# Performance work log

Hardware: AMD Instinct MI355X
Metric: run time of the kernel (lower is better)

Reference implementation:

```python
import jax, jax.numpy as jnp
import numpy as np

EPS = 1e-3  # Keras LayerNormalization default epsilon


def layernorm(x, g, b):
    mu = jnp.mean(x, axis=-1, keepdims=True)
    var = jnp.var(x, axis=-1, keepdims=True)
    return (x - mu) * jax.lax.rsqrt(var + EPS) * g + b


def setup_inputs() -> dict:
    key = jax.random.key(0)
    ks = jax.random.split(key, 16)
    B, T, C = 2, 2048, 1024
    F = 4 * C
    std = 0.02
    inp = {
        "x": jax.random.normal(ks[0], (B, T, C), jnp.float32),
        "ln1_g": jnp.ones((C,), jnp.float32),
        "ln1_b": jnp.zeros((C,), jnp.float32),
        "Wq": std * jax.random.normal(ks[1], (C, C), jnp.float32),
        "bq": jnp.zeros((C,), jnp.float32),
        "Wk": std * jax.random.normal(ks[2], (C, C), jnp.float32),
        "bk": jnp.zeros((C,), jnp.float32),
        "Wv": std * jax.random.normal(ks[3], (C, C), jnp.float32),
        "bv": jnp.zeros((C,), jnp.float32),
        "ln2_g": jnp.ones((C,), jnp.float32),
        "ln2_b": jnp.zeros((C,), jnp.float32),
        "W1": std * jax.random.normal(ks[4], (C, F), jnp.float32),
        "b1": jnp.zeros((F,), jnp.float32),
        "W2": std * jax.random.normal(ks[5], (F, C), jnp.float32),
        "b2": jnp.zeros((C,), jnp.float32),
    }
    return inp


N_HEADS = 16


def reference(x, ln1_g, ln1_b, Wq, bq, Wk, bk, Wv, bv, ln2_g, ln2_b, W1, b1, W2, b2):
    B, T, C = x.shape
    H = N_HEADS
    D = C // H

    h = layernorm(x, ln1_g, ln1_b)
    # [B,T,C] -> [B,H,T,D]
    def split_heads(y):
        return y.reshape(B, T, H, D).transpose(0, 2, 1, 3)

    q = split_heads(h @ Wq + bq)
    k = split_heads(h @ Wk + bk)
    v = split_heads(h @ Wv + bv)

    # Faithful to original: scores = K @ Q^T, i.e. scores[i,j] = k_i . q_j
    scores = jnp.einsum("bhid,bhjd->bhij", k, q) / jnp.sqrt(jnp.float32(D))
    causal = jnp.tril(jnp.ones((T, T), bool))  # [T,T]
    scores = jnp.where(causal[None, None], scores, -jnp.inf)
    w = jax.nn.softmax(scores, axis=-1)
    attn = jnp.einsum("bhij,bhjd->bhid", w, v)  # [B,H,T,D]
    attn = attn.transpose(0, 2, 1, 3).reshape(B, T, C)
    x = x + attn

    h2 = layernorm(x, ln2_g, ln2_b)
    ffn = jax.nn.gelu(h2 @ W1 + b1, approximate=False) @ W2 + b2
    x = x + ffn
    return x
```

## Files before the change

### kernel.cpp

```cpp
#include <hip/hip_runtime.h>
#include <hip/hip_bf16.h>
#include <math.h>

typedef __hip_bfloat16 bf16;
typedef __attribute__((ext_vector_type(8))) short bf16x8;
typedef __attribute__((ext_vector_type(4))) float f32x4;

__device__ __forceinline__ unsigned short f2bf_rne(float f) {
  unsigned u = __float_as_uint(f);
  u += 0x7fffu + ((u >> 16) & 1u);
  return (unsigned short)(u >> 16);
}
__device__ __forceinline__ float bf2f(unsigned short s) {
  return __uint_as_float(((unsigned)s) << 16);
}

__device__ __forceinline__ float gelu_fast(float v) {
  float u = v * (0.7978845608f + 0.0356774081f * v * v);
  float t = __builtin_amdgcn_exp2f(u * 2.8853900818f);
  float r = __builtin_amdgcn_rcpf(t + 1.0f);
  return v - v * r;
}

#define GLOBAL_AS __attribute__((address_space(1)))
#define LDS_AS __attribute__((address_space(3)))
__device__ __forceinline__ void gl2lds16(const void* g, void* l) {
  __builtin_amdgcn_global_load_lds((const GLOBAL_AS void*)g, (LDS_AS void*)l, 16, 0, 0);
}

__global__ __launch_bounds__(256) void ln_kernel(const float* __restrict__ x,
                                                 const float* __restrict__ g,
                                                 const float* __restrict__ b,
                                                 bf16* __restrict__ h) {
  int row = blockIdx.x, t = threadIdx.x;
  const float4 xv = ((const float4*)(x + (size_t)row * 1024))[t];
  float s = xv.x + xv.y + xv.z + xv.w;
  float sq = xv.x * xv.x + xv.y * xv.y + xv.z * xv.z + xv.w * xv.w;
  #pragma unroll
  for (int m = 1; m < 64; m <<= 1) { s += __shfl_xor(s, m); sq += __shfl_xor(sq, m); }
  __shared__ float ps[4], pq[4];
  if ((t & 63) == 0) { ps[t >> 6] = s; pq[t >> 6] = sq; }
  __syncthreads();
  s = ps[0] + ps[1] + ps[2] + ps[3];
  sq = pq[0] + pq[1] + pq[2] + pq[3];
  float mean = s * (1.0f / 1024.0f);
  float var = sq * (1.0f / 1024.0f) - mean * mean;
  float rs = rsqrtf(var + 1e-3f);
  float4 gv = ((const float4*)g)[t];
  float4 bv = ((const float4*)b)[t];
  ushort4 o;
  o.x = f2bf_rne((xv.x - mean) * rs * gv.x + bv.x);
  o.y = f2bf_rne((xv.y - mean) * rs * gv.y + bv.y);
  o.z = f2bf_rne((xv.z - mean) * rs * gv.z + bv.z);
  o.w = f2bf_rne((xv.w - mean) * rs * gv.w + bv.w);
  ((ushort4*)(h + (size_t)row * 1024))[t] = o;
}

__device__ __forceinline__ void tr_tile(const float* __restrict__ W, bf16* __restrict__ WT,
                                        int R, int Cc, int bx, int by, int t) {
  __shared__ float tile[32][33];
  int tx = t & 31, ty = t >> 5;
  #pragma unroll
  for (int k = 0; k < 4; k++) {
    int rr = ty + k * 8;
    tile[rr][tx] = W[(size_t)(by + rr) * Cc + bx + tx];
  }
  __syncthreads();
  unsigned short* out = reinterpret_cast<unsigned short*>(WT);
  #pragma unroll
  for (int k = 0; k < 4; k++) {
    int rr = ty + k * 8;
    out[(size_t)(bx + rr) * R + by + tx] = f2bf_rne(tile[tx][rr]);
  }
}

__global__ __launch_bounds__(256) void transpose_all(const float* __restrict__ Wq,
                                                     const float* __restrict__ Wk,
                                                     const float* __restrict__ Wv,
                                                     const float* __restrict__ W1,
                                                     const float* __restrict__ W2,
                                                     bf16* __restrict__ WqkT,
                                                     bf16* __restrict__ W1T,
                                                     bf16* __restrict__ W2T) {
  int id = blockIdx.x, t = threadIdx.x;
  if (id < 3072) {
    int sect = id >> 10, r = id & 1023;
    const float* W = sect == 0 ? Wq : (sect == 1 ? Wk : Wv);
    bf16* WT = WqkT + (size_t)sect * 1048576;
    tr_tile(W, WT, 1024, 1024, (r & 31) * 32, (r >> 5) * 32, t);
  } else if (id < 7168) {
    int r = id - 3072;
    tr_tile(W1, W1T, 1024, 4096, (r & 127) * 32, (r >> 7) * 32, t);
  } else {
    int r = id - 7168;
    tr_tile(W2, W2T, 4096, 1024, (r & 31) * 32, (r >> 5) * 32, t);
  }
}

__device__ __forceinline__ void mainloop_256(const bf16* __restrict__ A,
                                             const bf16* __restrict__ BT,
                                             int lda, int nk, int m0, int n0,
                                             char* ldsb, int t,
                                             f32x4 (&acc)[8][4]) {
  const int lane = t & 63, wave = t >> 6;
  const int l = lane & 15, quad = lane >> 4;
  const int wm = (wave >> 2) * 128, wn = (wave & 3) * 64;
  const int srow = wave * 8 + (lane >> 3);
  const int scol = ((lane & 7) ^ (lane >> 3)) * 8;
  const int grp0 = (quad ^ (l & 7)) * 16;
  const int grp1 = ((4 + quad) ^ (l & 7)) * 16;

  bf16x8 a[4][2], b01[2][2], b23[2][2];

  auto stA = [&](int buf, int half, int kt) {
    const bf16* s = A + (size_t)(m0 + half * 128 + srow) * lda + kt * 64 + scol;
    char* d = ldsb + buf * 65536 + half * 16384 + wave * 1024;
    gl2lds16(s, d);
    gl2lds16(s + (size_t)64 * lda, d + 8192);
  };
  auto stB = [&](int buf, int half, int kt) {
    const bf16* s = BT + (size_t)(n0 + half * 128 + srow) * lda + kt * 64 + scol;
    char* d = ldsb + buf * 65536 + 32768 + half * 16384 + wave * 1024;
    gl2lds16(s, d);
    gl2lds16(s + (size_t)64 * lda, d + 8192);
  };
  auto rdA = [&](int buf, int mh) {
    const char* base = ldsb + buf * 65536 + (wm + mh * 64 + l) * 128;
    #pragma unroll
    for (int ii = 0; ii < 4; ii++) {
      a[ii][0] = *(const bf16x8*)(base + ii * 2048 + grp0);
      a[ii][1] = *(const bf16x8*)(base + ii * 2048 + grp1);
    }
  };
  auto rdB = [&](int buf, int nh, bf16x8 (&bb)[2][2]) {
    const char* base = ldsb + buf * 65536 + 32768 + (wn + nh * 32 + l) * 128;
    #pragma unroll
    for (int jj = 0; jj < 2; jj++) {
      bb[jj][0] = *(const bf16x8*)(base + jj * 2048 + grp0);
      bb[jj][1] = *(const bf16x8*)(base + jj * 2048 + grp1);
    }
  };
  auto mm4 = [&](int mi, bf16x8 (&bb)[2][2], int nj) {
    #pragma unroll
    for (int ii = 0; ii < 4; ii++)
      #pragma unroll
      for (int jj = 0; jj < 2; jj++) {
        acc[mi + ii][nj + jj] = __builtin_amdgcn_mfma_f32_16x16x32_bf16(
            a[ii][0], bb[jj][0], acc[mi + ii][nj + jj], 0, 0, 0);
        acc[mi + ii][nj + jj] = __builtin_amdgcn_mfma_f32_16x16x32_bf16(
            a[ii][1], bb[jj][1], acc[mi + ii][nj + jj], 0, 0, 0);
      }
  };

#define BARX() __builtin_amdgcn_s_barrier()
#define LGKM0() do { asm volatile("s_waitcnt lgkmcnt(0)" ::: "memory"); \
                     __builtin_amdgcn_sched_barrier(0); } while (0)
#define HALF4(BC, DOA, SAB, SAK, DOB, SBB, SBK, VMN)                      \
  do {                                                                    \
    rdA(BC, 0); rdB(BC, 0, b01);                                          \
    if (DOA) stA(SAB, 0, SAK);                                            \
    BARX(); LGKM0();                                                      \
    __builtin_amdgcn_s_setprio(1); mm4(0, b01, 0);                        \
    __builtin_amdgcn_s_setprio(0); BARX();                                \
    rdB(BC, 1, b23);                                                      \
    if (DOA) stA(SAB, 1, SAK);                                            \
    BARX(); LGKM0();                                                      \
    __builtin_amdgcn_s_setprio(1); mm4(0, b23, 2);                        \
    __builtin_amdgcn_s_setprio(0); BARX();                                \
    rdA(BC, 1);                                                           \
    if (DOB) stB(SBB, 0, SBK);                                            \
    BARX(); LGKM0();                                                      \
    __builtin_amdgcn_s_setprio(1); mm4(4, b01, 0);                        \
    __builtin_amdgcn_s_setprio(0); BARX();                                \
    if (DOB) stB(SBB, 1, SBK);                                            \
    BARX();                                                               \
    __builtin_amdgcn_s_setprio(1); mm4(4, b23, 2);                        \
    __builtin_amdgcn_s_setprio(0);                                        \
    asm volatile("s_waitcnt vmcnt(" VMN ")" ::: "memory");                \
    BARX();                                                               \
  } while (0)

  const int nt = nk >> 6;
  stA(0, 0, 0); stA(0, 1, 0);
  stB(0, 0, 0); stB(0, 1, 0);
  stB(1, 0, 1); stB(1, 1, 1);
  asm volatile("s_waitcnt vmcnt(4)" ::: "memory");
  BARX();
  int tt = 0;
  for (; tt + 2 < nt; tt += 2) {
    HALF4(0, 1, 1, tt + 1, 1, 0, tt + 2, "4");
    HALF4(1, 1, 0, tt + 2, 1, 1, tt + 3, "4");
  }
  HALF4(0, 1, 1, tt + 1, 0, 0, 0, "0");
  HALF4(1, 0, 0, 0, 0, 0, 0, "0");
#undef HALF4
#undef LGKM0
#undef BARX
}

__global__ __launch_bounds__(512, 2) void gemm_ffn1(const bf16* __restrict__ A,
                                                    const bf16* __restrict__ BT,
                                                    const float* __restrict__ bias,
                                                    bf16* __restrict__ out,
                                                    int N, int K) {
  extern __shared__ char lds[];
  int t = threadIdx.x;
  int n0 = blockIdx.x * 256, m0 = blockIdx.y * 256;
  f32x4 acc[8][4];
  #pragma unroll
  for (int i = 0; i < 8; i++)
    #pragma unroll
    for (int j = 0; j < 4; j++) acc[i][j] = (f32x4){0.f, 0.f, 0.f, 0.f};
  mainloop_256(A, BT, K, K, m0, n0, lds, t, acc);

  int lane = t & 63, wave = t >> 6;
  int l = lane & 15, quad = lane >> 4;
  int wm = (wave >> 2) * 128, wn = (wave & 3) * 64;
  int r4 = quad * 4;
  unsigned short* os = reinterpret_cast<unsigned short*>(out);
  #pragma unroll
  for (int i = 0; i < 8; i++)
    #pragma unroll
    for (int j = 0; j < 4; j++) {
      int col = n0 + wn + j * 16 + l;
      float bval = bias[col];
      #pragma unroll
      for (int r = 0; r < 4; r++) {
        int row = m0 + wm + i * 16 + r4 + r;
        os[(size_t)row * N + col] = f2bf_rne(gelu_fast(acc[i][j][r] + bval));
      }
    }
}

__global__ __launch_bounds__(512, 2) void gemm_ffn2(const bf16* __restrict__ A,
                                                    const bf16* __restrict__ BT,
                                                    unsigned short* __restrict__ p0,
                                                    unsigned short* __restrict__ p1,
                                                    unsigned short* __restrict__ p2,
                                                    unsigned short* __restrict__ p3) {
  extern __shared__ char lds[];
  int t = threadIdx.x;
  int n0 = blockIdx.x * 256, m0 = blockIdx.y * 256;
  int z = blockIdx.z;
  f32x4 acc[8][4];
  #pragma unroll
  for (int i = 0; i < 8; i++)
    #pragma unroll
    for (int j = 0; j < 4; j++) acc[i][j] = (f32x4){0.f, 0.f, 0.f, 0.f};
  mainloop_256(A + z * 1024, BT + z * 1024, 4096, 1024, m0, n0, lds, t, acc);

  unsigned short* p = z == 0 ? p0 : (z == 1 ? p1 : (z == 2 ? p2 : p3));
  int lane = t & 63, wave = t >> 6;
  int l = lane & 15, quad = lane >> 4;
  int wm = (wave >> 2) * 128, wn = (wave & 3) * 64;
  int r4 = quad * 4;
  #pragma unroll
  for (int i = 0; i < 8; i++)
    #pragma unroll
    for (int j = 0; j < 4; j++) {
      int col = n0 + wn + j * 16 + l;
      #pragma unroll
      for (int r = 0; r < 4; r++) {
        int row = m0 + wm + i * 16 + r4 + r;
        p[(size_t)row * 1024 + col] = f2bf_rne(acc[i][j][r]);
      }
    }
}

__global__ __launch_bounds__(256) void reduce_ffn2(const unsigned short* __restrict__ p0,
                                                   const unsigned short* __restrict__ p1,
                                                   const unsigned short* __restrict__ p2,
                                                   const unsigned short* __restrict__ p3,
                                                   const float* __restrict__ x1,
                                                   const float* __restrict__ bias,
                                                   float* __restrict__ out) {
  int row = blockIdx.x, t = threadIdx.x;
  size_t base = (size_t)row * 1024;
  ushort4 a = ((const ushort4*)(p0 + base))[t];
  ushort4 b = ((const ushort4*)(p1 + base))[t];
  ushort4 c = ((const ushort4*)(p2 + base))[t];
  ushort4 d = ((const ushort4*)(p3 + base))[t];
  float4 xv = ((const float4*)(x1 + base))[t];
  float4 bv = ((const float4*)bias)[t];
  float4 o;
  o.x = (bf2f(a.x) + bf2f(b.x)) + (bf2f(c.x) + bf2f(d.x)) + xv.x + bv.x;
  o.y = (bf2f(a.y) + bf2f(b.y)) + (bf2f(c.y) + bf2f(d.y)) + xv.y + bv.y;
  o.z = (bf2f(a.z) + bf2f(b.z)) + (bf2f(c.z) + bf2f(d.z)) + xv.z + bv.z;
  o.w = (bf2f(a.w) + bf2f(b.w)) + (bf2f(c.w) + bf2f(d.w)) + xv.w + bv.w;
  ((float4*)(out + base))[t] = o;
}

__global__ __launch_bounds__(512, 2) void gemm_qkv(const bf16* __restrict__ A,
                                                   const bf16* __restrict__ BT,
                                                   const float* __restrict__ bq,
                                                   const float* __restrict__ bk,
                                                   const float* __restrict__ bv,
                                                   bf16* __restrict__ qb,
                                                   bf16* __restrict__ kb,
                                                   bf16* __restrict__ vt,
                                                   int K) {
  extern __shared__ char lds[];
  int t = threadIdx.x;
  int n0 = blockIdx.x * 256, m0 = blockIdx.y * 256;
  f32x4 acc[8][4];
  #pragma unroll
  for (int i = 0; i < 8; i++)
    #pragma unroll
    for (int j = 0; j < 4; j++) acc[i][j] = (f32x4){0.f, 0.f, 0.f, 0.f};
  mainloop_256(A, BT, K, K, m0, n0, lds, t, acc);

  int lane = t & 63, wave = t >> 6;
  int l = lane & 15, quad = lane >> 4;
  int wm = (wave >> 2) * 128, wn = (wave & 3) * 64;
  int sect = n0 >> 10;
  const float* bias = sect == 0 ? bq : (sect == 1 ? bk : bv);
  int r4 = quad * 4;
  #pragma unroll
  for (int i = 0; i < 8; i++)
    #pragma unroll
    for (int j = 0; j < 4; j++) {
      int col = n0 + wn + j * 16 + l;
      int c1 = col & 1023;
      float bval = bias[c1];
      int row0 = m0 + wm + i * 16 + r4;
      if (sect < 2) {
        bf16* o = sect == 0 ? qb : kb;
        unsigned short* os = reinterpret_cast<unsigned short*>(o);
        #pragma unroll
        for (int r = 0; r < 4; r++)
          os[(size_t)(row0 + r) * 1024 + c1] = f2bf_rne(acc[i][j][r] + bval);
      } else {
        int hh = c1 >> 6, d = c1 & 63;
        int b = row0 >> 11, t0 = row0 & 2047;
        ushort4 pk;
        pk.x = f2bf_rne(acc[i][j][0] + bval);
        pk.y = f2bf_rne(acc[i][j][1] + bval);
        pk.z = f2bf_rne(acc[i][j][2] + bval);
        pk.w = f2bf_rne(acc[i][j][3] + bval);
        *(ushort4*)((unsigned short*)vt + (size_t)((b * 16 + hh) * 64 + d) * 2048 + t0) = pk;
      }
    }
}

__global__ __launch_bounds__(256) void attn_mfma(const bf16* __restrict__ qb,
                                                 const bf16* __restrict__ kb,
                                                 const bf16* __restrict__ vt,
                                                 const float* __restrict__ x,
                                                 float* __restrict__ x1) {
  __shared__ bf16 QP[64][72];
  __shared__ bf16 KV[2][2][64][64];
  int t = threadIdx.x;
  int bh = blockIdx.x;
  int b = bh >> 4, h = bh & 15;
  size_t qk_base = (size_t)b * 2048 * 1024 + (size_t)h * 64;
  size_t vt_base = (size_t)bh * 64 * 2048;
  int lane = t & 63, wave = t >> 6;
  int l = lane & 15, quad = lane >> 4;
  int sw = l & 7;
  int srow8 = lane >> 3;
  int scol = ((lane & 7) ^ srow8) * 8;
  const float cs = 0.125f * 1.44269504088896f;
  int y = blockIdx.y;

  for (int pass = 0; pass < 2; pass++) {
    int it = pass ? 31 - y : y;
    int i0 = it * 64;
    int njt = it + 1;
    __syncthreads();
    #pragma unroll
    for (int c0 = 0; c0 < 512; c0 += 256) {
      int c = c0 + t;
      int row = c >> 3, col8 = (c & 7) * 8;
      *(uint4*)&QP[row][col8] = *(const uint4*)(kb + qk_base + (size_t)(i0 + row) * 1024 + col8);
    }
    #pragma unroll
    for (int c = 0; c < 2; c++) {
      int rr = wave * 16 + c * 8 + srow8;
      gl2lds16(qb + qk_base + (size_t)rr * 1024 + scol,
               (char*)KV + wave * 2048 + c * 1024);
      gl2lds16(vt + vt_base + (size_t)rr * 2048 + scol,
               (char*)KV + 8192 + wave * 2048 + c * 1024);
    }
    __syncthreads();

    bf16x8 qf0 = *(const bf16x8*)&QP[wave * 16 + l][quad * 8];
    bf16x8 qf1 = *(const bf16x8*)&QP[wave * 16 + l][32 + quad * 8];
    float lsum = 0.f;
    f32x4 Oacc[4];
    #pragma unroll
    for (int dt = 0; dt < 4; dt++) Oacc[dt] = (f32x4){0.f, 0.f, 0.f, 0.f};
    int iblk = i0 + wave * 16;

    int buf = 0;
    for (int jt = 0; jt < njt; jt++) {
      int j0v = jt * 64;
      if (jt + 1 < njt) {
        int j1 = j0v + 64;
        #pragma unroll
        for (int c = 0; c < 2; c++) {
          int rr = wave * 16 + c * 8 + srow8;
          gl2lds16(qb + qk_base + (size_t)(j1 + rr) * 1024 + scol,
                   (char*)KV + (buf ^ 1) * 16384 + wave * 2048 + c * 1024);
          gl2lds16(vt + vt_base + (size_t)rr * 2048 + j1 + scol,
                   (char*)KV + (buf ^ 1) * 16384 + 8192 + wave * 2048 + c * 1024);
        }
      }

      const bf16* Kb = &KV[buf][0][0][0];
      #pragma unroll
      for (int nt = 0; nt < 4; nt++) {
        int jb = j0v + nt * 16;
        uint2 pk;
        if (jb > iblk + 15) {
          pk.x = 0u; pk.y = 0u;
        } else {
          const bf16* kr = Kb + (nt * 16 + l) * 64;
          bf16x8 kf0 = *(const bf16x8*)(kr + ((quad ^ sw) * 8));
          bf16x8 kf1 = *(const bf16x8*)(kr + (((4 + quad) ^ sw) * 8));
          f32x4 sv = (f32x4){0.f, 0.f, 0.f, 0.f};
          sv = __builtin_amdgcn_mfma_f32_16x16x32_bf16(kf0, qf0, sv, 0, 0, 0);
          sv = __builtin_amdgcn_mfma_f32_16x16x32_bf16(kf1, qf1, sv, 0, 0, 0);
          float p0, p1, p2, p3;
          if (jb + 15 <= iblk) {
            p0 = __builtin_amdgcn_exp2f(sv[0] * cs);
            p1 = __builtin_amdgcn_exp2f(sv[1] * cs);
            p2 = __builtin_amdgcn_exp2f(sv[2] * cs);
            p3 = __builtin_amdgcn_exp2f(sv[3] * cs);
          } else {
            int i_ = iblk + l, jbase = jb + quad * 4;
            p0 = (jbase + 0 > i_) ? 0.f : __builtin_amdgcn_exp2f(sv[0] * cs);
            p1 = (jbase + 1 > i_) ? 0.f : __builtin_amdgcn_exp2f(sv[1] * cs);
            p2 = (jbase + 2 > i_) ? 0.f : __builtin_amdgcn_exp2f(sv[2] * cs);
            p3 = (jbase + 3 > i_) ? 0.f : __builtin_amdgcn_exp2f(sv[3] * cs);
          }
          lsum += (p0 + p1) + (p2 + p3);
          union { __hip_bfloat162 h2; unsigned u; } c0u, c1u;
          c0u.h2 = __float22bfloat162_rn(make_float2(p0, p1));
          c1u.h2 = __float22bfloat162_rn(make_float2(p2, p3));
          pk.x = c0u.u; pk.y = c1u.u;
        }
        *(uint2*)&QP[wave * 16 + l][nt * 16 + quad * 4] = pk;
      }
      asm volatile("s_waitcnt lgkmcnt(0)" ::: "memory");

      bf16x8 ap0 = *(const bf16x8*)&QP[wave * 16 + l][quad * 8];
      bf16x8 ap1 = *(const bf16x8*)&QP[wave * 16 + l][32 + quad * 8];
      const bf16* Vb = &KV[buf][1][0][0];
      #pragma unroll
      for (int dt = 0; dt < 4; dt++) {
        const bf16* vr = Vb + (dt * 16 + l) * 64;
        bf16x8 bv0 = *(const bf16x8*)(vr + ((quad ^ sw) * 8));
        bf16x8 bv1 = *(const bf16x8*)(vr + (((4 + quad) ^ sw) * 8));
        Oacc[dt] = __builtin_amdgcn_mfma_f32_16x16x32_bf16(ap0, bv0, Oacc[dt], 0, 0, 0);
        Oacc[dt] = __builtin_amdgcn_mfma_f32_16x16x32_bf16(ap1, bv1, Oacc[dt], 0, 0, 0);
      }
      __syncthreads();
      buf ^= 1;
    }

    lsum += __shfl_xor(lsum, 16);
    lsum += __shfl_xor(lsum, 32);
    #pragma unroll
    for (int r = 0; r < 4; r++) {
      float lv = __shfl(lsum, quad * 4 + r);
      float inv = 1.0f / lv;
      int row = i0 + wave * 16 + quad * 4 + r;
      size_t gi = qk_base + (size_t)row * 1024;
      #pragma unroll
      for (int dt = 0; dt < 4; dt++) {
        int d = dt * 16 + l;
        x1[gi + d] = x[gi + d] + Oacc[dt][r] * inv;
      }
    }
  }
}

extern "C" void kernel_launch(void* const* d_in, const int* in_sizes, int n_in,
                              void* d_out, int out_size, void* d_ws, size_t ws_size,
                              hipStream_t stream) {
  const float* x    = (const float*)d_in[0];
  const float* ln1g = (const float*)d_in[1];
  const float* ln1b = (const float*)d_in[2];
  const float* Wq   = (const float*)d_in[3];
  const float* bq   = (const float*)d_in[4];
  const float* Wk   = (const float*)d_in[5];
  const float* bk   = (const float*)d_in[6];
  const float* Wv   = (const float*)d_in[7];
  const float* bv   = (const float*)d_in[8];
  const float* ln2g = (const float*)d_in[9];
  const float* ln2b = (const float*)d_in[10];
  const float* W1   = (const float*)d_in[11];
  const float* b1   = (const float*)d_in[12];
  const float* W2   = (const float*)d_in[13];
  const float* b2   = (const float*)d_in[14];

  char* ws = (char*)d_ws;
  float* x1  = (float*)(ws + 0);
  bf16* h    = (bf16*)(ws + 16777216);
  bf16* WqkT = (bf16*)(ws + 25165824);
  bf16* W1T  = (bf16*)(ws + 31457280);
  bf16* W2T  = (bf16*)(ws + 39845888);
  bf16* qb   = (bf16*)(ws + 48234496);
  bf16* kb   = (bf16*)(ws + 56623104);
  bf16* vt   = (bf16*)(ws + 65011712);
  bf16* act  = (bf16*)(ws + 73400320);

  static bool s_attr_done = false;
  if (!s_attr_done) {
    hipFuncSetAttribute(reinterpret_cast<const void*>(gemm_qkv),
                        hipFuncAttributeMaxDynamicSharedMemorySize, 131072);
    hipFuncSetAttribute(reinterpret_cast<const void*>(gemm_ffn1),
                        hipFuncAttributeMaxDynamicSharedMemorySize, 131072);
    hipFuncSetAttribute(reinterpret_cast<const void*>(gemm_ffn2),
                        hipFuncAttributeMaxDynamicSharedMemorySize, 131072);
    s_attr_done = true;
  }

  transpose_all<<<11264, 256, 0, stream>>>(Wq, Wk, Wv, W1, W2, WqkT, W1T, W2T);
  ln_kernel<<<4096, 256, 0, stream>>>(x, ln1g, ln1b, h);
  gemm_qkv<<<dim3(12, 16), 512, 131072, stream>>>(h, WqkT, bq, bk, bv, qb, kb, vt, 1024);
  attn_mfma<<<dim3(32, 16), 256, 0, stream>>>(qb, kb, vt, x, x1);
  ln_kernel<<<4096, 256, 0, stream>>>(x1, ln2g, ln2b, h);
  gemm_ffn1<<<dim3(16, 16), 512, 131072, stream>>>(h, W1T, b1, act, 4096, 1024);
  gemm_ffn2<<<dim3(4, 16, 4), 512, 131072, stream>>>(act, W2T,
      (unsigned short*)qb, (unsigned short*)kb, (unsigned short*)vt, (unsigned short*)h);
  reduce_ffn2<<<4096, 256, 0, stream>>>((const unsigned short*)qb, (const unsigned short*)kb,
                                        (const unsigned short*)vt, (const unsigned short*)h,
                                        x1, b2, (float*)d_out);
}
```

Before: 291.4 us.

## Run both attention passes concurrently in 512-thread blocks, reading K/V from global

The attention kernel now uses 512 threads, so its two query-tile passes (y and 31-y) run concurrently in separate wave groups instead of one after another. The shared K/V double buffer and every block-wide barrier are gone. Each wave loads K and V fragments straight from global memory (relying on L1/L2) and keeps only a private P tile in LDS. On the diagonal tile, waves skip the upper-half V MFMA that is fully masked. The trade is more global-load traffic and cache pressure in exchange for no synchronisation, and the loads are no longer staged with a swizzle.

```diff
diff --git a/kernel.cpp b/kernel.cpp
--- a/kernel.cpp
+++ b/kernel.cpp
@@ -342,13 +342,12 @@
     }
 }
 
-__global__ __launch_bounds__(256) void attn_mfma(const bf16* __restrict__ qb,
-                                                 const bf16* __restrict__ kb,
-                                                 const bf16* __restrict__ vt,
-                                                 const float* __restrict__ x,
-                                                 float* __restrict__ x1) {
-  __shared__ bf16 QP[64][72];
-  __shared__ bf16 KV[2][2][64][64];
+__global__ __launch_bounds__(512, 4) void attn_mfma(const bf16* __restrict__ qb,
+                                                    const bf16* __restrict__ kb,
+                                                    const bf16* __restrict__ vt,
+                                                    const float* __restrict__ x,
+                                                    float* __restrict__ x1) {
+  __shared__ bf16 P[8][16][68];
   int t = threadIdx.x;
   int bh = blockIdx.x;
   int b = bh >> 4, h = bh & 15;
@@ -356,121 +355,98 @@
   size_t vt_base = (size_t)bh * 64 * 2048;
   int lane = t & 63, wave = t >> 6;
   int l = lane & 15, quad = lane >> 4;
-  int sw = l & 7;
-  int srow8 = lane >> 3;
-  int scol = ((lane & 7) ^ srow8) * 8;
   const float cs = 0.125f * 1.44269504088896f;
   int y = blockIdx.y;
-
-  for (int pass = 0; pass < 2; pass++) {
-    int it = pass ? 31 - y : y;
-    int i0 = it * 64;
-    int njt = it + 1;
-    __syncthreads();
-    #pragma unroll
-    for (int c0 = 0; c0 < 512; c0 += 256) {
-      int c = c0 + t;
-      int row = c >> 3, col8 = (c & 7) * 8;
-      *(uint4*)&QP[row][col8] = *(const uint4*)(kb + qk_base + (size_t)(i0 + row) * 1024 + col8);
-    }
-    #pragma unroll
-    for (int c = 0; c < 2; c++) {
-      int rr = wave * 16 + c * 8 + srow8;
-      gl2lds16(qb + qk_base + (size_t)rr * 1024 + scol,
-               (char*)KV + wave * 2048 + c * 1024);
-      gl2lds16(vt + vt_base + (size_t)rr * 2048 + scol,
-               (char*)KV + 8192 + wave * 2048 + c * 1024);
-    }
-    __syncthreads();
-
-    bf16x8 qf0 = *(const bf16x8*)&QP[wave * 16 + l][quad * 8];
-    bf16x8 qf1 = *(const bf16x8*)&QP[wave * 16 + l][32 + quad * 8];
-    float lsum = 0.f;
-    f32x4 Oacc[4];
-    #pragma unroll
-    for (int dt = 0; dt < 4; dt++) Oacc[dt] = (f32x4){0.f, 0.f, 0.f, 0.f};
-    int iblk = i0 + wave * 16;
-
-    int buf = 0;
-    for (int jt = 0; jt < njt; jt++) {
-      int j0v = jt * 64;
-      if (jt + 1 < njt) {
-        int j1 = j0v + 64;
-        #pragma unroll
-        for (int c = 0; c < 2; c++) {
-          int rr = wave * 16 + c * 8 + srow8;
-          gl2lds16(qb + qk_base + (size_t)(j1 + rr) * 1024 + scol,
-                   (char*)KV + (buf ^ 1) * 16384 + wave * 2048 + c * 1024);
-          gl2lds16(vt + vt_base + (size_t)rr * 2048 + j1 + scol,
-                   (char*)KV + (buf ^ 1) * 16384 + 8192 + wave * 2048 + c * 1024);
+  int half = wave >> 2, w4 = wave & 3;
+  int it = half ? 31 - y : y;
+  int i0 = it * 64;
+  int iblk = i0 + w4 * 16;
+  int njt = it + 1;
+
+  const bf16* qrow = kb + qk_base + (size_t)(iblk + l) * 1024;
+  bf16x8 qf0 = *(const bf16x8*)(qrow + quad * 8);
+  bf16x8 qf1 = *(const bf16x8*)(qrow + 32 + quad * 8);
+
+  float lsum = 0.f;
+  f32x4 Oacc[4];
+  #pragma unroll
+  for (int dt = 0; dt < 4; dt++) Oacc[dt] = (f32x4){0.f, 0.f, 0.f, 0.f};
+
+  bf16 (*Pw)[68] = P[wave];
+
+  for (int jt = 0; jt < njt; jt++) {
+    int j0v = jt * 64;
+    const bf16* Kb = qb + qk_base + (size_t)j0v * 1024;
+    #pragma unroll
+    for (int nt = 0; nt < 4; nt++) {
+      int jb = j0v + nt * 16;
+      uint2 pk;
+      if (jb > iblk + 15) {
+        pk.x = 0u; pk.y = 0u;
+      } else {
+        const bf16* kr = Kb + (size_t)(nt * 16 + l) * 1024;
+        bf16x8 kf0 = *(const bf16x8*)(kr + quad * 8);
+        bf16x8 kf1 = *(const bf16x8*)(kr + 32 + quad * 8);
+        f32x4 sv = (f32x4){0.f, 0.f, 0.f, 0.f};
+        sv = __builtin_amdgcn_mfma_f32_16x16x32_bf16(kf0, qf0, sv, 0, 0, 0);
+        sv = __builtin_amdgcn_mfma_f32_16x16x32_bf16(kf1, qf1, sv, 0, 0, 0);
+        float p0, p1, p2, p3;
+        if (jb + 15 <= iblk) {
+          p0 = __builtin_amdgcn_exp2f(sv[0] * cs);
+          p1 = __builtin_amdgcn_exp2f(sv[1] * cs);
+          p2 = __builtin_amdgcn_exp2f(sv[2] * cs);
+          p3 = __builtin_amdgcn_exp2f(sv[3] * cs);
+        } else {
+          int i_ = iblk + l, jbase = jb + quad * 4;
+          p0 = (jbase + 0 > i_) ? 0.f : __builtin_amdgcn_exp2f(sv[0] * cs);
+          p1 = (jbase + 1 > i_) ? 0.f : __builtin_amdgcn_exp2f(sv[1] * cs);
+          p2 = (jbase + 2 > i_) ? 0.f : __builtin_amdgcn_exp2f(sv[2] * cs);
+          p3 = (jbase + 3 > i_) ? 0.f : __builtin_amdgcn_exp2f(sv[3] * cs);
         }
-      }
-
-      const bf16* Kb = &KV[buf][0][0][0];
-      #pragma unroll
-      for (int nt = 0; nt < 4; nt++) {
-        int jb = j0v + nt * 16;
-        uint2 pk;
-        if (jb > iblk + 15) {
-          pk.x = 0u; pk.y = 0u;
-        } else {
-          const bf16* kr = Kb + (nt * 16 + l) * 64;
-          bf16x8 kf0 = *(const bf16x8*)(kr + ((quad ^ sw) * 8));
-          bf16x8 kf1 = *(const bf16x8*)(kr + (((4 + quad) ^ sw) * 8));
-          f32x4 sv = (f32x4){0.f, 0.f, 0.f, 0.f};
-          sv = __builtin_amdgcn_mfma_f32_16x16x32_bf16(kf0, qf0, sv, 0, 0, 0);
-          sv = __builtin_amdgcn_mfma_f32_16x16x32_bf16(kf1, qf1, sv, 0, 0, 0);
-          float p0, p1, p2, p3;
-          if (jb + 15 <= iblk) {
-            p0 = __builtin_amdgcn_exp2f(sv[0] * cs);
-            p1 = __builtin_amdgcn_exp2f(sv[1] * cs);
-            p2 = __builtin_amdgcn_exp2f(sv[2] * cs);
-            p3 = __builtin_amdgcn_exp2f(sv[3] * cs);
-          } else {
-            int i_ = iblk + l, jbase = jb + quad * 4;
-            p0 = (jbase + 0 > i_) ? 0.f : __builtin_amdgcn_exp2f(sv[0] * cs);
-            p1 = (jbase + 1 > i_) ? 0.f : __builtin_amdgcn_exp2f(sv[1] * cs);
-            p2 = (jbase + 2 > i_) ? 0.f : __builtin_amdgcn_exp2f(sv[2] * cs);
-            p3 = (jbase + 3 > i_) ? 0.f : __builtin_amdgcn_exp2f(sv[3] * cs);
-          }
-          lsum += (p0 + p1) + (p2 + p3);
-          union { __hip_bfloat162 h2; unsigned u; } c0u, c1u;
-          c0u.h2 = __float22bfloat162_rn(make_float2(p0, p1));
-          c1u.h2 = __float22bfloat162_rn(make_float2(p2, p3));
-          pk.x = c0u.u; pk.y = c1u.u;
-        }
-        *(uint2*)&QP[wave * 16 + l][nt * 16 + quad * 4] = pk;
-      }
-      asm volatile("s_waitcnt lgkmcnt(0)" ::: "memory");
-
-      bf16x8 ap0 = *(const bf16x8*)&QP[wave * 16 + l][quad * 8];
-      bf16x8 ap1 = *(const bf16x8*)&QP[wave * 16 + l][32 + quad * 8];
-      const bf16* Vb = &KV[buf][1][0][0];
+        lsum += (p0 + p1) + (p2 + p3);
+        union { __hip_bfloat162 h2; unsigned u; } c0u, c1u;
+        c0u.h2 = __float22bfloat162_rn(make_float2(p0, p1));
+        c1u.h2 = __float22bfloat162_rn(make_float2(p2, p3));
+        pk.x = c0u.u; pk.y = c1u.u;
+      }
+      *(uint2*)&Pw[l][nt * 16 + quad * 4] = pk;
+    }
+    asm volatile("s_waitcnt lgkmcnt(0)" ::: "memory");
+
+    bf16x8 ap0 = *(const bf16x8*)&Pw[l][quad * 8];
+    const bf16* Vb = vt + vt_base + j0v;
+    if ((jt < it) || (w4 >= 2)) {
+      bf16x8 ap1 = *(const bf16x8*)&Pw[l][32 + quad * 8];
       #pragma unroll
       for (int dt = 0; dt < 4; dt++) {
-        const bf16* vr = Vb + (dt * 16 + l) * 64;
-        bf16x8 bv0 = *(const bf16x8*)(vr + ((quad ^ sw) * 8));
-        bf16x8 bv1 = *(const bf16x8*)(vr + (((4 + quad) ^ sw) * 8));
+        const bf16* vr = Vb + (size_t)(dt * 16 + l) * 2048;
+        bf16x8 bv0 = *(const bf16x8*)(vr + quad * 8);
+        bf16x8 bv1 = *(const bf16x8*)(vr + 32 + quad * 8);
         Oacc[dt] = __builtin_amdgcn_mfma_f32_16x16x32_bf16(ap0, bv0, Oacc[dt], 0, 0, 0);
         Oacc[dt] = __builtin_amdgcn_mfma_f32_16x16x32_bf16(ap1, bv1, Oacc[dt], 0, 0, 0);
       }
-      __syncthreads();
-      buf ^= 1;
-    }
-
-    lsum += __shfl_xor(lsum, 16);
-    lsum += __shfl_xor(lsum, 32);
-    #pragma unroll
-    for (int r = 0; r < 4; r++) {
-      float lv = __shfl(lsum, quad * 4 + r);
-      float inv = 1.0f / lv;
-      int row = i0 + wave * 16 + quad * 4 + r;
-      size_t gi = qk_base + (size_t)row * 1024;
+    } else {
       #pragma unroll
       for (int dt = 0; dt < 4; dt++) {
-        int d = dt * 16 + l;
-        x1[gi + d] = x[gi + d] + Oacc[dt][r] * inv;
-      }
+        const bf16* vr = Vb + (size_t)(dt * 16 + l) * 2048;
+        bf16x8 bv0 = *(const bf16x8*)(vr + quad * 8);
+        Oacc[dt] = __builtin_amdgcn_mfma_f32_16x16x32_bf16(ap0, bv0, Oacc[dt], 0, 0, 0);
+      }
+    }
+  }
+
+  lsum += __shfl_xor(lsum, 16);
+  lsum += __shfl_xor(lsum, 32);
+  #pragma unroll
+  for (int r = 0; r < 4; r++) {
+    float lv = __shfl(lsum, quad * 4 + r);
+    float inv = 1.0f / lv;
+    int row = iblk + quad * 4 + r;
+    size_t gi = qk_base + (size_t)row * 1024;
+    #pragma unroll
+    for (int dt = 0; dt < 4; dt++) {
+      int d = dt * 16 + l;
+      x1[gi + d] = x[gi + d] + Oacc[dt][r] * inv;
     }
   }
 }
@@ -519,7 +495,7 @@
   transpose_all<<<11264, 256, 0, stream>>>(Wq, Wk, Wv, W1, W2, WqkT, W1T, W2T);
   ln_kernel<<<4096, 256, 0, stream>>>(x, ln1g, ln1b, h);
   gemm_qkv<<<dim3(12, 16), 512, 131072, stream>>>(h, WqkT, bq, bk, bv, qb, kb, vt, 1024);
-  attn_mfma<<<dim3(32, 16), 256, 0, stream>>>(qb, kb, vt, x, x1);
+  attn_mfma<<<dim3(32, 16), 512, 0, stream>>>(qb, kb, vt, x, x1);
   ln_kernel<<<4096, 256, 0, stream>>>(x1, ln2g, ln2b, h);
   gemm_ffn1<<<dim3(16, 16), 512, 131072, stream>>>(h, W1T, b1, act, 4096, 1024);
   gemm_ffn2<<<dim3(4, 16, 4), 512, 131072, stream>>>(act, W2T,
```

Measured after the change: 374.7 us. +28.6%, slower.

## Split attention row-tile pairs into separate blocks with heavy-first ordering and swizzled LDS

Applied to the files above, without the earlier changes.

Previously each attention block processed two query tiles (it and 31-it) in sequence for load balance. Now each block handles one tile, launched on a 32x32 grid, with the mapping ordering long causal tiles first so heavy blocks start early. The Q/P shared buffer drops its padding and uses an XOR swizzle, Q is loaded with async global-to-LDS copies, and launch bounds request 4 blocks per CU for higher occupancy. The cost is more blocks with uneven work, relying on the scheduler to balance them.

```diff
diff --git a/kernel.cpp b/kernel.cpp
--- a/kernel.cpp
+++ b/kernel.cpp
@@ -342,12 +342,12 @@
     }
 }
 
-__global__ __launch_bounds__(256) void attn_mfma(const bf16* __restrict__ qb,
-                                                 const bf16* __restrict__ kb,
-                                                 const bf16* __restrict__ vt,
-                                                 const float* __restrict__ x,
-                                                 float* __restrict__ x1) {
-  __shared__ bf16 QP[64][72];
+__global__ __launch_bounds__(256, 4) void attn_mfma(const bf16* __restrict__ qb,
+                                                    const bf16* __restrict__ kb,
+                                                    const bf16* __restrict__ vt,
+                                                    const float* __restrict__ x,
+                                                    float* __restrict__ x1) {
+  __shared__ bf16 QP[64][64];
   __shared__ bf16 KV[2][2][64][64];
   int t = threadIdx.x;
   int bh = blockIdx.x;
@@ -361,116 +361,113 @@
   int scol = ((lane & 7) ^ srow8) * 8;
   const float cs = 0.125f * 1.44269504088896f;
   int y = blockIdx.y;
-
-  for (int pass = 0; pass < 2; pass++) {
-    int it = pass ? 31 - y : y;
-    int i0 = it * 64;
-    int njt = it + 1;
+  int yr = y & 7, yk = y >> 3;
+  int it = yk == 0 ? 31 - yr : (yk == 1 ? 16 + yr : (yk == 2 ? 15 - yr : yr));
+  int i0 = it * 64;
+  int njt = it + 1;
+  int iblk = i0 + wave * 16;
+
+  #pragma unroll
+  for (int c = 0; c < 2; c++) {
+    int rr = wave * 16 + c * 8 + srow8;
+    gl2lds16(kb + qk_base + (size_t)(i0 + rr) * 1024 + scol,
+             (char*)QP + wave * 2048 + c * 1024);
+    gl2lds16(qb + qk_base + (size_t)rr * 1024 + scol,
+             (char*)KV + wave * 2048 + c * 1024);
+    gl2lds16(vt + vt_base + (size_t)rr * 2048 + scol,
+             (char*)KV + 8192 + wave * 2048 + c * 1024);
+  }
+  __syncthreads();
+
+  const char* qr = (const char*)&QP[wave * 16 + l][0];
+  bf16x8 qf0 = *(const bf16x8*)(qr + ((quad ^ sw) * 16));
+  bf16x8 qf1 = *(const bf16x8*)(qr + (((4 + quad) ^ sw) * 16));
+  float lsum = 0.f;
+  f32x4 Oacc[4];
+  #pragma unroll
+  for (int dt = 0; dt < 4; dt++) Oacc[dt] = (f32x4){0.f, 0.f, 0.f, 0.f};
+
+  char* Pw = (char*)&QP[wave * 16 + l][0];
+
+  int buf = 0;
+  for (int jt = 0; jt < njt; jt++) {
+    int j0v = jt * 64;
+    if (jt + 1 < njt) {
+      int j1 = j0v + 64;
+      #pragma unroll
+      for (int c = 0; c < 2; c++) {
+        int rr = wave * 16 + c * 8 + srow8;
+        gl2lds16(qb + qk_base + (size_t)(j1 + rr) * 1024 + scol,
+                 (char*)KV + (buf ^ 1) * 16384 + wave * 2048 + c * 1024);
+        gl2lds16(vt + vt_base + (size_t)rr * 2048 + j1 + scol,
+                 (char*)KV + (buf ^ 1) * 16384 + 8192 + wave * 2048 + c * 1024);
+      }
+    }
+
+    const bf16* Kb = &KV[buf][0][0][0];
+    #pragma unroll
+    for (int nt = 0; nt < 4; nt++) {
+      int jb = j0v + nt * 16;
+      uint2 pk;
+      if (jb > iblk + 15) {
+        pk.x = 0u; pk.y = 0u;
+      } else {
+        const bf16* kr = Kb + (nt * 16 + l) * 64;
+        bf16x8 kf0 = *(const bf16x8*)(kr + ((quad ^ sw) * 8));
+        bf16x8 kf1 = *(const bf16x8*)(kr + (((4 + quad) ^ sw) * 8));
+        f32x4 sv = (f32x4){0.f, 0.f, 0.f, 0.f};
+        sv = __builtin_amdgcn_mfma_f32_16x16x32_bf16(kf0, qf0, sv, 0, 0, 0);
+        sv = __builtin_amdgcn_mfma_f32_16x16x32_bf16(kf1, qf1, sv, 0, 0, 0);
+        float p0, p1, p2, p3;
+        if (jb + 15 <= iblk) {
+          p0 = __builtin_amdgcn_exp2f(sv[0] * cs);
+          p1 = __builtin_amdgcn_exp2f(sv[1] * cs);
+          p2 = __builtin_amdgcn_exp2f(sv[2] * cs);
+          p3 = __builtin_amdgcn_exp2f(sv[3] * cs);
+        } else {
+          int i_ = iblk + l, jbase = jb + quad * 4;
+          p0 = (jbase + 0 > i_) ? 0.f : __builtin_amdgcn_exp2f(sv[0] * cs);
+          p1 = (jbase + 1 > i_) ? 0.f : __builtin_amdgcn_exp2f(sv[1] * cs);
+          p2 = (jbase + 2 > i_) ? 0.f : __builtin_amdgcn_exp2f(sv[2] * cs);
+          p3 = (jbase + 3 > i_) ? 0.f : __builtin_amdgcn_exp2f(sv[3] * cs);
+        }
+        lsum += (p0 + p1) + (p2 + p3);
+        union { __hip_bfloat162 h2; unsigned u; } c0u, c1u;
+        c0u.h2 = __float22bfloat162_rn(make_float2(p0, p1));
+        c1u.h2 = __float22bfloat162_rn(make_float2(p2, p3));
+        pk.x = c0u.u; pk.y = c1u.u;
+      }
+      *(uint2*)(Pw + (((nt * 2 + (quad >> 1)) ^ sw) << 4) + ((quad & 1) << 3)) = pk;
+    }
+    asm volatile("s_waitcnt lgkmcnt(0)" ::: "memory");
+
+    bf16x8 ap0 = *(const bf16x8*)(Pw + ((quad ^ sw) << 4));
+    bf16x8 ap1 = *(const bf16x8*)(Pw + (((4 + quad) ^ sw) << 4));
+    const bf16* Vb = &KV[buf][1][0][0];
+    #pragma unroll
+    for (int dt = 0; dt < 4; dt++) {
+      const bf16* vr = Vb + (dt * 16 + l) * 64;
+      bf16x8 bv0 = *(const bf16x8*)(vr + ((quad ^ sw) * 8));
+      bf16x8 bv1 = *(const bf16x8*)(vr + (((4 + quad) ^ sw) * 8));
+      Oacc[dt] = __builtin_amdgcn_mfma_f32_16x16x32_bf16(ap0, bv0, Oacc[dt], 0, 0, 0);
+      Oacc[dt] = __builtin_amdgcn_mfma_f32_16x16x32_bf16(ap1, bv1, Oacc[dt], 0, 0, 0);
+    }
     __syncthreads();
-    #pragma unroll
-    for (int c0 = 0; c0 < 512; c0 += 256) {
-      int c = c0 + t;
-      int row = c >> 3, col8 = (c & 7) * 8;
-      *(uint4*)&QP[row][col8] = *(const uint4*)(kb + qk_base + (size_t)(i0 + row) * 1024 + col8);
-    }
-    #pragma unroll
-    for (int c = 0; c < 2; c++) {
-      int rr = wave * 16 + c * 8 + srow8;
-      gl2lds16(qb + qk_base + (size_t)rr * 1024 + scol,
-               (char*)KV + wave * 2048 + c * 1024);
-      gl2lds16(vt + vt_base + (size_t)rr * 2048 + scol,
-               (char*)KV + 8192 + wave * 2048 + c * 1024);
-    }
-    __syncthreads();
-
-    bf16x8 qf0 = *(const bf16x8*)&QP[wave * 16 + l][quad * 8];
-    bf16x8 qf1 = *(const bf16x8*)&QP[wave * 16 + l][32 + quad * 8];
-    float lsum = 0.f;
-    f32x4 Oacc[4];
-    #pragma unroll
-    for (int dt = 0; dt < 4; dt++) Oacc[dt] = (f32x4){0.f, 0.f, 0.f, 0.f};
-    int iblk = i0 + wave * 16;
-
-    int buf = 0;
-    for (int jt = 0; jt < njt; jt++) {
-      int j0v = jt * 64;
-      if (jt + 1 < njt) {
-        int j1 = j0v + 64;
-        #pragma unroll
-        for (int c = 0; c < 2; c++) {
-          int rr = wave * 16 + c * 8 + srow8;
-          gl2lds16(qb + qk_base + (size_t)(j1 + rr) * 1024 + scol,
-                   (char*)KV + (buf ^ 1) * 16384 + wave * 2048 + c * 1024);
-          gl2lds16(vt + vt_base + (size_t)rr * 2048 + j1 + scol,
-                   (char*)KV + (buf ^ 1) * 16384 + 8192 + wave * 2048 + c * 1024);
-        }
-      }
-
-      const bf16* Kb = &KV[buf][0][0][0];
-      #pragma unroll
-      for (int nt = 0; nt < 4; nt++) {
-        int jb = j0v + nt * 16;
-        uint2 pk;
-        if (jb > iblk + 15) {
-          pk.x = 0u; pk.y = 0u;
-        } else {
-          const bf16* kr = Kb + (nt * 16 + l) * 64;
-          bf16x8 kf0 = *(const bf16x8*)(kr + ((quad ^ sw) * 8));
-          bf16x8 kf1 = *(const bf16x8*)(kr + (((4 + quad) ^ sw) * 8));
-          f32x4 sv = (f32x4){0.f, 0.f, 0.f, 0.f};
-          sv = __builtin_amdgcn_mfma_f32_16x16x32_bf16(kf0, qf0, sv, 0, 0, 0);
-          sv = __builtin_amdgcn_mfma_f32_16x16x32_bf16(kf1, qf1, sv, 0, 0, 0);
-          float p0, p1, p2, p3;
-          if (jb + 15 <= iblk) {
-            p0 = __builtin_amdgcn_exp2f(sv[0] * cs);
-            p1 = __builtin_amdgcn_exp2f(sv[1] * cs);
-            p2 = __builtin_amdgcn_exp2f(sv[2] * cs);
-            p3 = __builtin_amdgcn_exp2f(sv[3] * cs);
-          } else {
-            int i_ = iblk + l, jbase = jb + quad * 4;
-            p0 = (jbase + 0 > i_) ? 0.f : __builtin_amdgcn_exp2f(sv[0] * cs);
-            p1 = (jbase + 1 > i_) ? 0.f : __builtin_amdgcn_exp2f(sv[1] * cs);
-            p2 = (jbase + 2 > i_) ? 0.f : __builtin_amdgcn_exp2f(sv[2] * cs);
-            p3 = (jbase + 3 > i_) ? 0.f : __builtin_amdgcn_exp2f(sv[3] * cs);
-          }
-          lsum += (p0 + p1) + (p2 + p3);
-          union { __hip_bfloat162 h2; unsigned u; } c0u, c1u;
-          c0u.h2 = __float22bfloat162_rn(make_float2(p0, p1));
-          c1u.h2 = __float22bfloat162_rn(make_float2(p2, p3));
-          pk.x = c0u.u; pk.y = c1u.u;
-        }
-        *(uint2*)&QP[wave * 16 + l][nt * 16 + quad * 4] = pk;
-      }
-      asm volatile("s_waitcnt lgkmcnt(0)" ::: "memory");
-
-      bf16x8 ap0 = *(const bf16x8*)&QP[wave * 16 + l][quad * 8];
-      bf16x8 ap1 = *(const bf16x8*)&QP[wave * 16 + l][32 + quad * 8];
-      const bf16* Vb = &KV[buf][1][0][0];
-      #pragma unroll
-      for (int dt = 0; dt < 4; dt++) {
-        const bf16* vr = Vb + (dt * 16 + l) * 64;
-        bf16x8 bv0 = *(const bf16x8*)(vr + ((quad ^ sw) * 8));
-        bf16x8 bv1 = *(const bf16x8*)(vr + (((4 + quad) ^ sw) * 8));
-        Oacc[dt] = __builtin_amdgcn_mfma_f32_16x16x32_bf16(ap0, bv0, Oacc[dt], 0, 0, 0);
-        Oacc[dt] = __builtin_amdgcn_mfma_f32_16x16x32_bf16(ap1, bv1, Oacc[dt], 0, 0, 0);
-      }
-      __syncthreads();
-      buf ^= 1;
-    }
-
-    lsum += __shfl_xor(lsum, 16);
-    lsum += __shfl_xor(lsum, 32);
-    #pragma unroll
-    for (int r = 0; r < 4; r++) {
-      float lv = __shfl(lsum, quad * 4 + r);
-      float inv = 1.0f / lv;
-      int row = i0 + wave * 16 + quad * 4 + r;
-      size_t gi = qk_base + (size_t)row * 1024;
-      #pragma unroll
-      for (int dt = 0; dt < 4; dt++) {
-        int d = dt * 16 + l;
-        x1[gi + d] = x[gi + d] + Oacc[dt][r] * inv;
-      }
+    buf ^= 1;
+  }
+
+  lsum += __shfl_xor(lsum, 16);
+  lsum += __shfl_xor(lsum, 32);
+  #pragma unroll
+  for (int r = 0; r < 4; r++) {
+    float lv = __shfl(lsum, quad * 4 + r);
+    float inv = 1.0f / lv;
+    int row = iblk + quad * 4 + r;
+    size_t gi = qk_base + (size_t)row * 1024;
+    #pragma unroll
+    for (int dt = 0; dt < 4; dt++) {
+      int d = dt * 16 + l;
+      x1[gi + d] = x[gi + d] + Oacc[dt][r] * inv;
     }
   }
 }
@@ -519,7 +516,7 @@
   transpose_all<<<11264, 256, 0, stream>>>(Wq, Wk, Wv, W1, W2, WqkT, W1T, W2T);
   ln_kernel<<<4096, 256, 0, stream>>>(x, ln1g, ln1b, h);
   gemm_qkv<<<dim3(12, 16), 512, 131072, stream>>>(h, WqkT, bq, bk, bv, qb, kb, vt, 1024);
-  attn_mfma<<<dim3(32, 16), 256, 0, stream>>>(qb, kb, vt, x, x1);
+  attn_mfma<<<dim3(32, 32), 256, 0, stream>>>(qb, kb, vt, x, x1);
   ln_kernel<<<4096, 256, 0, stream>>>(x1, ln2g, ln2b, h);
   gemm_ffn1<<<dim3(16, 16), 512, 131072, stream>>>(h, W1T, b1, act, 4096, 1024);
   gemm_ffn2<<<dim3(4, 16, 4), 512, 131072, stream>>>(act, W2T,
```

Measured after the change: 295.9 us. About the same (+1.6%).
